# Performance work log

Hardware: AMD Instinct MI355X
Metric: run time of the kernel (lower is better)

The kernel has to match this reference:

```python
import jax, jax.numpy as jnp
import numpy as np

N = 50000      # nodes
E = 400000     # edges (before self-loops)
IN = 256       # in_dim
H = 4          # heads in layer 1
C = 64         # h_dim (per-head channels, layer 1)
OUT = 16       # out_dim (layer 2, 1 head)
NEG_SLOPE = 0.2


def gatv2_layer(x, src, dst, Wl, bl, Wr, br, att, bias, heads, ch, concat, num_nodes):
    # x: [N, F]; src/dst: [E']; Wl/Wr: [F, heads*ch]; att: [heads, ch]
    xl = (x @ Wl + bl).reshape(num_nodes, heads, ch)  # source transform
    xr = (x @ Wr + br).reshape(num_nodes, heads, ch)  # target transform
    m = xl[src] + xr[dst]                              # [E', H, C] gather
    e = jnp.sum(jax.nn.leaky_relu(m, NEG_SLOPE) * att, axis=-1)  # [E', H]
    # segment softmax over incoming edges of each dst node (self-loops ensure non-empty)
    emax = jax.ops.segment_max(e, dst, num_segments=num_nodes)   # [N, H]
    ee = jnp.exp(e - emax[dst])
    denom = jax.ops.segment_sum(ee, dst, num_segments=num_nodes)  # [N, H]
    alpha = ee / (denom[dst] + 1e-16)                              # [E', H]
    out = jax.ops.segment_sum(alpha[..., None] * xl[src], dst, num_segments=num_nodes)  # [N,H,C]
    if concat:
        out = out.reshape(num_nodes, heads * ch)
    else:
        out = out.mean(axis=1)
    return out + bias


def setup_inputs() -> dict:
    key = jax.random.key(0)
    ks = jax.random.split(key, 16)
    s = 0.05
    inp = {
        "x": jax.random.normal(ks[0], (N, IN), jnp.float32),
        "edge_index": jax.random.randint(ks[1], (2, E), 0, N),
        # layer 1 params (in_dim -> heads*h_dim)
        "Wl1": jax.random.normal(ks[2], (IN, H * C), jnp.float32) * s,
        "bl1": jnp.zeros((H * C,), jnp.float32),
        "Wr1": jax.random.normal(ks[3], (IN, H * C), jnp.float32) * s,
        "br1": jnp.zeros((H * C,), jnp.float32),
        "att1": jax.random.normal(ks[4], (H, C), jnp.float32) * s,
        "bias1": jnp.zeros((H * C,), jnp.float32),
        # layer 2 params (heads*h_dim -> out_dim, 1 head)
        "Wl2": jax.random.normal(ks[5], (H * C, OUT), jnp.float32) * s,
        "bl2": jnp.zeros((OUT,), jnp.float32),
        "Wr2": jax.random.normal(ks[6], (H * C, OUT), jnp.float32) * s,
        "br2": jnp.zeros((OUT,), jnp.float32),
        "att2": jax.random.normal(ks[7], (1, OUT), jnp.float32) * s,
        "bias2": jnp.zeros((OUT,), jnp.float32),
    }
    return inp


def reference(x, edge_index, Wl1, bl1, Wr1, br1, att1, bias1, Wl2, bl2, Wr2, br2, att2, bias2):
    # add self loops (PyG GATv2Conv default add_self_loops=True)
    loop = jnp.arange(N, dtype=edge_index.dtype)
    src = jnp.concatenate([edge_index[0], loop])
    dst = jnp.concatenate([edge_index[1], loop])
    h = gatv2_layer(x, src, dst, Wl1, bl1, Wr1, br1, att1, bias1, H, C, True, N)
    h = jnp.tanh(h)
    o = gatv2_layer(h, src, dst, Wl2, bl2, Wr2, br2, att2, bias2, 1, OUT, False, N)
    return o, jax.nn.log_softmax(o, axis=1)
```

## Files before the change

kernel.cpp:

```cpp
#include <hip/hip_runtime.h>

typedef __bf16 bfv8 __attribute__((ext_vector_type(8)));
typedef float f32x4 __attribute__((ext_vector_type(4)));
typedef float f32x2 __attribute__((ext_vector_type(2)));
typedef short shortv8 __attribute__((ext_vector_type(8)));
typedef unsigned short usv8 __attribute__((ext_vector_type(8)));

__device__ __forceinline__ float b2f(unsigned short u) {
  unsigned int v = ((unsigned int)u) << 16;
  float f;
  __builtin_memcpy(&f, &v, 4);
  return f;
}
__device__ __forceinline__ unsigned short f2b(float f) {
  unsigned int u;
  __builtin_memcpy(&u, &f, 4);
  u += 0x7fffu + ((u >> 16) & 1u);
  return (unsigned short)(u >> 16);
}

__device__ __forceinline__ f32x2 bf2x(unsigned int u) {
  f32x2 r;
  r.x = __builtin_bit_cast(float, u << 16);
  r.y = __builtin_bit_cast(float, u & 0xffff0000u);
  return r;
}

template <int CTRL>
__device__ __forceinline__ float dpp_mv(float x) {
  int xi = __builtin_bit_cast(int, x);
  int yi = __builtin_amdgcn_update_dpp(0, xi, CTRL, 0xf, 0xf, true);
  return __builtin_bit_cast(float, yi);
}

__device__ __forceinline__ float tanh_fast(float x) {
  float e2 = __expf(2.f * x);
  float r = __builtin_amdgcn_rcpf(e2 + 1.f);
  float th = fmaf(-2.f, r, 1.f);
  if (!(th == th)) th = 0.f;
  return th;
}

__global__ void probe_kernel(const unsigned short* __restrict__ x, int* __restrict__ flag) {
  int lane = threadIdx.x;
  int cnt = 0;
  for (int i = lane; i < 4096; i += 64) {
    unsigned int e = (x[i] >> 7) & 0xffu;
    if (e >= 0x86u) cnt++;
  }
#pragma unroll
  for (int off = 1; off < 64; off <<= 1) cnt += __shfl_xor(cnt, off, 64);
  if (lane == 0) *flag = (cnt > 100) ? 1 : 0;
}

#define P_TOT 140352
__global__ __launch_bounds__(256) void fused_pre_kernel(
    const void* __restrict__ x, unsigned short* __restrict__ Xc,
    const int* __restrict__ flagp, int NX,
    const int* __restrict__ ei, int E, int Nn, int* __restrict__ cnt,
    const void* p0, const void* p1, const void* p2, const void* p3,
    const void* p4, const void* p5, const void* p6, const void* p7,
    const void* p8, const void* p9, const void* p10, const void* p11,
    unsigned short* __restrict__ Pc, int nb_convx, int nb_count) {
  int b = blockIdx.x;
  int t = threadIdx.x;
  if (b < nb_convx) {
    if (!*flagp) return;
    int i = (b * 256 + t) * 4;
    if (i >= NX) return;
    float4 f = *reinterpret_cast<const float4*>((const float*)x + i);
    ushort4 o;
    o.x = f2b(f.x); o.y = f2b(f.y); o.z = f2b(f.z); o.w = f2b(f.w);
    *reinterpret_cast<ushort4*>(Xc + i) = o;
  } else if (b < nb_convx + nb_count) {
    int i = (b - nb_convx) * 256 + t;
    int total = E + Nn;
    if (i >= total) return;
    int d = (i < E) ? ei[E + i] : (i - E);
    if ((unsigned)d >= (unsigned)Nn) d = 0;
    atomicAdd(&cnt[d], 1);
  } else {
    int i = (b - nb_convx - nb_count) * 256 + t;
    if (i >= P_TOT) return;
    const int offs[13] = {0, 65536, 65792, 131328, 131584, 131840, 132096,
                          136192, 136208, 140304, 140320, 140336, P_TOT};
    const void* ptrs[12] = {p0, p1, p2, p3, p4, p5, p6, p7, p8, p9, p10, p11};
    int flag = *flagp;
    int k = 0;
    while (i >= offs[k + 1]) k++;
    int local = i - offs[k];
    unsigned short v;
    if (flag) v = f2b(((const float*)ptrs[k])[local]);
    else v = ((const unsigned short*)ptrs[k])[local];
    Pc[i] = v;
  }
}

__global__ __launch_bounds__(1024) void fused_mid_kernel(
    const int* __restrict__ cnt, int* __restrict__ row_start, int* __restrict__ blkTot,
    int* __restrict__ cursor, int Nn, int nb_scan,
    const unsigned short* __restrict__ Pc,
    unsigned short* __restrict__ WT1, unsigned short* __restrict__ WT2) {
  int b = blockIdx.x;
  int t = threadIdx.x;
  if (b < nb_scan) {
    __shared__ int buf[1024];
    int i = b * 1024 + t;
    int v = (i < Nn) ? cnt[i] : 0;
    buf[t] = v;
    if (i < Nn) cursor[i] = 0;
    __syncthreads();
    for (int off = 1; off < 1024; off <<= 1) {
      int x = (t >= off) ? buf[t - off] : 0;
      __syncthreads();
      buf[t] += x;
      __syncthreads();
    }
    if (i < Nn) row_start[i] = buf[t] - v;
    if (t == 1023) blkTot[b] = buf[1023];
  } else {
    int idx = (b - nb_scan) * 1024 + t;
    if (idx < 512 * 256) {
      int n = idx >> 8, k = idx & 255;
      WT1[idx] = (n < 256) ? Pc[0 + k * 256 + n]
                           : Pc[65792 + k * 256 + (n - 256)];
    } else {
      int j = idx - 512 * 256;
      if (j < 32 * 256) {
        int n = j >> 8, k = j & 255;
        WT2[j] = (n < 16) ? Pc[132096 + k * 16 + n]
                          : Pc[136208 + k * 16 + (n - 16)];
      }
    }
  }
}

__global__ __launch_bounds__(64) void scan2_kernel(const int* __restrict__ blkTot,
                                                   int* __restrict__ blkOff, int nb,
                                                   int* __restrict__ row_start, int Nn,
                                                   int total) {
  int lane = threadIdx.x;
  int v = (lane < nb) ? blkTot[lane] : 0;
  int s = v;
#pragma unroll
  for (int off = 1; off < 64; off <<= 1) {
    int u = __shfl_up(s, off, 64);
    if (lane >= off) s += u;
  }
  int excl = s - v;
  blkOff[lane] = excl;
  if (lane == 63) blkOff[64] = s;
  int idx = Nn >> 10;
  int bo = (idx >= 64) ? __shfl(s, 63, 64) : __shfl(excl, idx, 64);
  if (lane == 0) row_start[Nn] = total - bo;
}

__global__ __launch_bounds__(256) void fill_kernel(const int* __restrict__ ei, int E, int Nn,
                                                   const int* __restrict__ row_start,
                                                   const int* __restrict__ blkOff,
                                                   int* __restrict__ cursor,
                                                   int* __restrict__ csr_src) {
  int i = blockIdx.x * 256 + threadIdx.x;
  int total = E + Nn;
  if (i >= total) return;
  int s, d;
  if (i < E) { s = ei[i]; d = ei[E + i]; } else { s = i - E; d = i - E; }
  if ((unsigned)d >= (unsigned)Nn) d = 0;
  if ((unsigned)s >= (unsigned)Nn) s = 0;
  int pos = row_start[d] + blkOff[d >> 10] + atomicAdd(&cursor[d], 1);
  if ((unsigned)pos < (unsigned)total) csr_src[pos] = s;
}

__global__ __launch_bounds__(256) void gemm1_kernel(
    const unsigned short* __restrict__ Xc,
    const unsigned short* __restrict__ x_raw,
    const int* __restrict__ flagp,
    const unsigned short* __restrict__ WT,
    const unsigned short* __restrict__ bl, const unsigned short* __restrict__ br,
    unsigned short* __restrict__ C, int M) {
  __shared__ unsigned short smem[16384];
  const unsigned short* X = (*flagp) ? Xc : x_raw;
  const int t = threadIdx.x;
  const int lane = t & 63;
  const int w = t >> 6;
  const int quad = lane >> 4;
  const int l16 = lane & 15;

  const int G = (M + 127) >> 7;
  const int nfull = (G >> 3) << 5;
  int bid = blockIdx.x, grp, n_blk;
  if (bid < nfull) {
    grp = (bid >> 5) * 8 + (bid & 7);
    n_blk = (bid >> 3) & 3;
  } else {
    int r = bid - nfull;
    grp = (G & ~7) + (r >> 2);
    n_blk = r & 3;
  }
  const int m_blk = grp * 128;
  const int m_base = m_blk + (w >> 1) * 64;
  const int n_base = n_blk * 128 + (w & 1) * 64;

  const int st_row = t >> 3;
  const int st_seg = t & 7;

  f32x4 acc[4][4];
#pragma unroll
  for (int i = 0; i < 4; i++)
#pragma unroll
    for (int j = 0; j < 4; j++) acc[i][j] = (f32x4){0.f, 0.f, 0.f, 0.f};

  shortv8 st[4];
#pragma unroll
  for (int i = 0; i < 4; i++) {
    int gr = m_blk + st_row + 32 * i;
    if (gr >= M) gr = M - 1;
    st[i] = *reinterpret_cast<const shortv8*>(X + (size_t)gr * 256 + st_seg * 8);
  }
#pragma unroll
  for (int i = 0; i < 4; i++) {
    int row = st_row + 32 * i;
    *reinterpret_cast<shortv8*>(smem + row * 64 + ((st_seg ^ (row & 7)) * 8)) = st[i];
  }
  __syncthreads();

#pragma unroll
  for (int c = 0; c < 4; c++) {
    if (c < 3) {
#pragma unroll
      for (int i = 0; i < 4; i++) {
        int gr = m_blk + st_row + 32 * i;
        if (gr >= M) gr = M - 1;
        st[i] = *reinterpret_cast<const shortv8*>(X + (size_t)gr * 256 + (c + 1) * 64 +
                                                  st_seg * 8);
      }
    }
    const unsigned short* bb = smem + (c & 1) * 8192;
#pragma unroll
    for (int sub = 0; sub < 2; sub++) {
      bfv8 a[4], b[4];
      int seg_r = sub * 4 + quad;
#pragma unroll
      for (int i = 0; i < 4; i++) {
        int lrow = (w >> 1) * 64 + 16 * i + l16;
        a[i] = *reinterpret_cast<const bfv8*>(bb + lrow * 64 + ((seg_r ^ (lrow & 7)) * 8));
      }
#pragma unroll
      for (int j = 0; j < 4; j++) {
        int col = n_base + 16 * j + l16;
        b[j] = *reinterpret_cast<const bfv8*>(WT + (size_t)col * 256 + c * 64 + sub * 32 +
                                              quad * 8);
      }
#pragma unroll
      for (int i = 0; i < 4; i++)
#pragma unroll
        for (int j = 0; j < 4; j++)
          acc[i][j] = __builtin_amdgcn_mfma_f32_16x16x32_bf16(a[i], b[j], acc[i][j], 0, 0, 0);
    }
    if (c < 3) {
      int buf = (c + 1) & 1;
#pragma unroll
      for (int i = 0; i < 4; i++) {
        int row = st_row + 32 * i;
        *reinterpret_cast<shortv8*>(smem + buf * 8192 + row * 64 +
                                    ((st_seg ^ (row & 7)) * 8)) = st[i];
      }
      __syncthreads();
    }
  }

  __syncthreads();
  unsigned short* lt = smem + w * 2304;
#pragma unroll
  for (int h = 0; h < 2; h++) {
#pragma unroll
    for (int j = 0; j < 4; j++) {
      int col = n_base + 16 * j + l16;
      float bias = (col < 256) ? b2f(bl[col]) : b2f(br[col - 256]);
#pragma unroll
      for (int i2 = 0; i2 < 2; i2++) {
        int i = 2 * h + i2;
#pragma unroll
        for (int r = 0; r < 4; r++)
          lt[(16 * i2 + quad * 4 + r) * 72 + 16 * j + l16] = f2b(acc[i][j][r] + bias);
      }
    }
#pragma unroll
    for (int pass = 0; pass < 4; pass++) {
      int row = pass * 8 + (lane >> 3);
      int colg = (lane & 7) * 8;
      shortv8 v = *reinterpret_cast<const shortv8*>(lt + row * 72 + colg);
      int grow = m_base + 32 * h + row;
      if (grow < M)
        *reinterpret_cast<shortv8*>(C + (size_t)grow * 512 + n_base + colg) = v;
    }
  }
}

__global__ __launch_bounds__(256) void gemm2_kernel(
    const unsigned short* __restrict__ H, const unsigned short* __restrict__ WT,
    const unsigned short* __restrict__ bl, const unsigned short* __restrict__ br,
    float* __restrict__ C, int M) {
  __shared__ unsigned short smem[8192];
  const int t = threadIdx.x;
  const int lane = t & 63;
  const int w = t >> 6;
  const int quad = lane >> 4;
  const int l16 = lane & 15;
  const int m_blk = blockIdx.x * 64;
  const int wrow = w * 16;

  const int st_row = t >> 2;
  const int st_seg = t & 3;

  f32x4 acc[2];
  acc[0] = (f32x4){0.f, 0.f, 0.f, 0.f};
  acc[1] = (f32x4){0.f, 0.f, 0.f, 0.f};

  int gr = m_blk + st_row;
  if (gr >= M) gr = M - 1;
  const unsigned short* hrow = H + (size_t)gr * 256;

  shortv8 st0 = *reinterpret_cast<const shortv8*>(hrow + st_seg * 8);
  shortv8 st1 = *reinterpret_cast<const shortv8*>(hrow + st_seg * 8 + 32);
  *reinterpret_cast<shortv8*>(smem + st_row * 64 + ((st_seg ^ (st_row & 7)) * 8)) = st0;
  *reinterpret_cast<shortv8*>(smem + st_row * 64 + (((st_seg + 4) ^ (st_row & 7)) * 8)) = st1;
  __syncthreads();

#pragma unroll
  for (int c = 0; c < 4; c++) {
    if (c < 3) {
      st0 = *reinterpret_cast<const shortv8*>(hrow + (c + 1) * 64 + st_seg * 8);
      st1 = *reinterpret_cast<const shortv8*>(hrow + (c + 1) * 64 + st_seg * 8 + 32);
    }
    const unsigned short* bb = smem + (c & 1) * 4096;
#pragma unroll
    for (int sub = 0; sub < 2; sub++) {
      int seg_r = sub * 4 + quad;
      int lrow = wrow + l16;
      bfv8 a = *reinterpret_cast<const bfv8*>(bb + lrow * 64 + ((seg_r ^ (lrow & 7)) * 8));
      bfv8 b[2];
#pragma unroll
      for (int j = 0; j < 2; j++) {
        int col = 16 * j + l16;
        b[j] = *reinterpret_cast<const bfv8*>(WT + (size_t)col * 256 + c * 64 + sub * 32 +
                                              quad * 8);
      }
#pragma unroll
      for (int j = 0; j < 2; j++)
        acc[j] = __builtin_amdgcn_mfma_f32_16x16x32_bf16(a, b[j], acc[j], 0, 0, 0);
    }
    if (c < 3) {
      int buf = (c + 1) & 1;
      *reinterpret_cast<shortv8*>(smem + buf * 4096 + st_row * 64 +
                                  ((st_seg ^ (st_row & 7)) * 8)) = st0;
      *reinterpret_cast<shortv8*>(smem + buf * 4096 + st_row * 64 +
                                  (((st_seg + 4) ^ (st_row & 7)) * 8)) = st1;
      __syncthreads();
    }
  }

#pragma unroll
  for (int j = 0; j < 2; j++) {
    int col = 16 * j + l16;
    float bias = (j == 0) ? b2f(bl[l16]) : b2f(br[l16]);
#pragma unroll
    for (int r = 0; r < 4; r++) {
      int row = m_blk + wrow + quad * 4 + r;
      if (row < M) C[(size_t)row * 32 + col] = acc[j][r] + bias;
    }
  }
}

__global__ __launch_bounds__(256) void agg1_kernel(
    const unsigned short* __restrict__ C1,
    const unsigned short* __restrict__ att1,
    const unsigned short* __restrict__ bias1,
    const int* __restrict__ row_start, const int* __restrict__ blkOff,
    const int* __restrict__ csr_src,
    unsigned short* __restrict__ H1,
    int Nn, int Etot) {
  int wid = blockIdx.x * 4 + (threadIdx.x >> 6);
  if (wid >= Nn) return;
  int lane = threadIdx.x & 63;
  int half = lane >> 5;
  int c0 = (lane & 31) * 8;

  f32x2 at2[4], xr2[4];
  {
    uint4 a4 = *reinterpret_cast<const uint4*>(att1 + c0);
    uint4 r4 = *reinterpret_cast<const uint4*>(C1 + (size_t)wid * 512 + 256 + c0);
    at2[0] = bf2x(a4.x); at2[1] = bf2x(a4.y); at2[2] = bf2x(a4.z); at2[3] = bf2x(a4.w);
    xr2[0] = bf2x(r4.x); xr2[1] = bf2x(r4.y); xr2[2] = bf2x(r4.z); xr2[3] = bf2x(r4.w);
  }

  float denom = 0.f;
  f32x2 acc2[4] = {};
  int beg = row_start[wid] + blkOff[wid >> 10];
  int end = row_start[wid + 1] + blkOff[(wid + 1) >> 10];
  if (beg < 0) beg = 0;
  if (end < beg || end - beg > Etot) end = beg;

  for (int base = beg; base < end; base += 64) {
    int cend = min(end, base + 64);
    int pl = base + lane;
    if (pl >= end) pl = end - 1;
    int s_pre = csr_src[pl];
#pragma unroll 4
    for (int i = base; i < cend; i += 2) {
      int p = i + half;
      bool valid = p < cend;
      int s = __shfl(s_pre, p - base, 64);
      if ((unsigned)s >= (unsigned)Nn) s = 0;
      uint4 rw = *reinterpret_cast<const uint4*>(C1 + (size_t)s * 512 + c0);
      f32x2 xl0 = bf2x(rw.x), xl1 = bf2x(rw.y), xl2 = bf2x(rw.z), xl3 = bf2x(rw.w);
      f32x2 m0 = xl0 + xr2[0], m1 = xl1 + xr2[1];
      f32x2 m2 = xl2 + xr2[2], m3 = xl3 + xr2[3];
      f32x2 l0 = __builtin_elementwise_max(m0, m0 * 0.2f);
      f32x2 l1 = __builtin_elementwise_max(m1, m1 * 0.2f);
      f32x2 l2 = __builtin_elementwise_max(m2, m2 * 0.2f);
      f32x2 l3 = __builtin_elementwise_max(m3, m3 * 0.2f);
      f32x2 d2 = l0 * at2[0];
      d2 += l1 * at2[1];
      d2 += l2 * at2[2];
      d2 += l3 * at2[3];
      float dot = d2.x + d2.y;
      dot += dpp_mv<0xB1>(dot);
      dot += dpp_mv<0x4E>(dot);
      dot += dpp_mv<0x141>(dot);
      dot = fminf(fmaxf(dot, -60.f), 60.f);
      float wgt = valid ? __expf(dot) : 0.f;
      denom += wgt;
      acc2[0] += xl0 * wgt;
      acc2[1] += xl1 * wgt;
      acc2[2] += xl2 * wgt;
      acc2[3] += xl3 * wgt;
    }
  }
  denom += __shfl_xor(denom, 32, 64);
#pragma unroll
  for (int k = 0; k < 4; k++) {
    acc2[k].x += __shfl_xor(acc2[k].x, 32, 64);
    acc2[k].y += __shfl_xor(acc2[k].y, 32, 64);
  }

  if (half == 0) {
    float inv = __builtin_amdgcn_rcpf(denom + 1e-16f);
    uint4 b4 = *reinterpret_cast<const uint4*>(bias1 + c0);
    f32x2 bb[4] = {bf2x(b4.x), bf2x(b4.y), bf2x(b4.z), bf2x(b4.w)};
    uint4 o;
    unsigned int od[4];
#pragma unroll
    for (int k = 0; k < 4; k++) {
      f32x2 xv = acc2[k] * inv + bb[k];
      float t0 = tanh_fast(xv.x);
      float t1 = tanh_fast(xv.y);
      od[k] = (unsigned int)f2b(t0) | ((unsigned int)f2b(t1) << 16);
    }
    o.x = od[0]; o.y = od[1]; o.z = od[2]; o.w = od[3];
    *reinterpret_cast<uint4*>(H1 + (size_t)wid * 256 + c0) = o;
  }
}

__global__ __launch_bounds__(256) void agg2_kernel(
    const float* __restrict__ C2,
    const unsigned short* __restrict__ att2,
    const unsigned short* __restrict__ bias2,
    const int* __restrict__ row_start, const int* __restrict__ blkOff,
    const int* __restrict__ csr_src,
    float* __restrict__ out,
    int Nn, int Etot) {
  int wid = blockIdx.x * 4 + (threadIdx.x >> 6);
  if (wid >= Nn) return;
  int lane = threadIdx.x & 63;
  int eslot = lane >> 2;
  int cg = (lane & 3) * 4;

  float at[4], xr[4];
  {
    ushort4 a4 = *reinterpret_cast<const ushort4*>(att2 + cg);
    at[0] = b2f(a4.x); at[1] = b2f(a4.y); at[2] = b2f(a4.z); at[3] = b2f(a4.w);
    float4 r4 = *reinterpret_cast<const float4*>(C2 + (size_t)wid * 32 + 16 + cg);
    xr[0] = r4.x; xr[1] = r4.y; xr[2] = r4.z; xr[3] = r4.w;
  }

  float denom = 0.f;
  float acc[4] = {0.f, 0.f, 0.f, 0.f};
  int beg = row_start[wid] + blkOff[wid >> 10];
  int end = row_start[wid + 1] + blkOff[(wid + 1) >> 10];
  if (beg < 0) beg = 0;
  if (end < beg || end - beg > Etot) end = beg;

  for (int base = beg; base < end; base += 64) {
    int cend = min(end, base + 64);
    int pl = base + lane;
    if (pl >= end) pl = end - 1;
    int s_pre = csr_src[pl];
    for (int i = base; i < cend; i += 16) {
      int p = i + eslot;
      bool valid = p < cend;
      int s = __shfl(s_pre, p - base, 64);
      if ((unsigned)s >= (unsigned)Nn) s = 0;
      float4 x4 = *reinterpret_cast<const float4*>(C2 + (size_t)s * 32 + cg);
      float xl[4] = {x4.x, x4.y, x4.z, x4.w};
      float dot = 0.f;
#pragma unroll
      for (int k = 0; k < 4; k++) {
        float m = xl[k] + xr[k];
        float l = fmaxf(m, 0.2f * m);
        dot = fmaf(l, at[k], dot);
      }
      dot += dpp_mv<0xB1>(dot);
      dot += dpp_mv<0x4E>(dot);
      dot = fminf(fmaxf(dot, -60.f), 60.f);
      float wgt = valid ? __expf(dot) : 0.f;
      denom += wgt;
#pragma unroll
      for (int k = 0; k < 4; k++) acc[k] = fmaf(wgt, xl[k], acc[k]);
    }
  }
  denom += dpp_mv<0x124>(denom);
  denom += dpp_mv<0x128>(denom);
#pragma unroll
  for (int k = 0; k < 4; k++) {
    acc[k] += dpp_mv<0x124>(acc[k]);
    acc[k] += dpp_mv<0x128>(acc[k]);
  }
#pragma unroll
  for (int off = 16; off <= 32; off <<= 1) {
    denom += __shfl_xor(denom, off, 64);
#pragma unroll
    for (int k = 0; k < 4; k++) acc[k] += __shfl_xor(acc[k], off, 64);
  }

  float inv = __builtin_amdgcn_rcpf(denom + 1e-16f);
  ushort4 b4 = *reinterpret_cast<const ushort4*>(bias2 + cg);
  float bb[4] = {b2f(b4.x), b2f(b4.y), b2f(b4.z), b2f(b4.w)};
  float o[4];
#pragma unroll
  for (int k = 0; k < 4; k++) {
    o[k] = acc[k] * inv + bb[k];
    if (!(o[k] == o[k])) o[k] = 0.f;
  }
  float mx = fmaxf(fmaxf(o[0], o[1]), fmaxf(o[2], o[3]));
  mx = fmaxf(mx, dpp_mv<0xB1>(mx));
  mx = fmaxf(mx, dpp_mv<0x4E>(mx));
  float se = 0.f;
#pragma unroll
  for (int k = 0; k < 4; k++) se += __expf(o[k] - mx);
  se += dpp_mv<0xB1>(se);
  se += dpp_mv<0x4E>(se);
  float ls = logf(se);
  if (lane < 4) {
    float4 vo = {o[0], o[1], o[2], o[3]};
    float4 vl = {o[0] - mx - ls, o[1] - mx - ls, o[2] - mx - ls, o[3] - mx - ls};
    *reinterpret_cast<float4*>(out + (size_t)wid * 16 + cg) = vo;
    *reinterpret_cast<float4*>(out + (size_t)Nn * 16 + (size_t)wid * 16 + cg) = vl;
  }
}

extern "C" void kernel_launch(void* const* d_in, const int* in_sizes, int n_in,
                              void* d_out, int out_size, void* d_ws, size_t ws_size,
                              hipStream_t stream) {
  const void* x_raw = d_in[0];
  const int* ei     = (const int*)d_in[1];

  const int M = in_sizes[0] / 256;
  const int E = in_sizes[1] / 2;
  const int TOT = E + M;
  const int NX = M * 256;

  char* ws = (char*)d_ws;
  size_t off = 0;
  auto alloc = [&](size_t bytes) -> void* {
    void* p = ws + off;
    off = (off + bytes + 255) & ~(size_t)255;
    return p;
  };
  int*            flag   = (int*)alloc(4);
  unsigned short* Pc     = (unsigned short*)alloc((size_t)P_TOT * 2);
  unsigned short* Xc     = (unsigned short*)alloc((size_t)NX * 2);
  unsigned short* WT1    = (unsigned short*)alloc((size_t)512 * 256 * 2);
  unsigned short* WT2    = (unsigned short*)alloc((size_t)32 * 256 * 2);
  int*            cnt    = (int*)alloc((size_t)M * 4);
  int*            cursor = (int*)alloc((size_t)M * 4);
  int*            row_start = (int*)alloc((size_t)(M + 1) * 4);
  int*            csr_src   = (int*)alloc((size_t)TOT * 4);
  int*            blkTot = (int*)alloc(64 * 4);
  int*            blkOff = (int*)alloc(65 * 4);
  float*          C2     = (float*)alloc((size_t)M * 32 * 4);
  unsigned short* C1     = (unsigned short*)alloc((size_t)M * 512 * 2);
  const size_t need = off;
  (void)n_in;
  unsigned short* H1 = Xc;

  if (ws_size < need) {
    hipMemsetAsync(d_out, 0, (size_t)out_size * 4, stream);
    return;
  }

  unsigned short* bl1c   = Pc + 65536;
  unsigned short* br1c   = Pc + 131328;
  unsigned short* att1c  = Pc + 131584;
  unsigned short* bias1c = Pc + 131840;
  unsigned short* bl2c   = Pc + 136192;
  unsigned short* br2c   = Pc + 140304;
  unsigned short* att2c  = Pc + 140320;
  unsigned short* bias2c = Pc + 140336;

  hipMemsetAsync(cnt, 0, (size_t)M * 4, stream);

  probe_kernel<<<1, 64, 0, stream>>>((const unsigned short*)x_raw, flag);

  const int nb_convx = (NX / 4 + 255) / 256;
  const int nb_count = (TOT + 255) / 256;
  const int nb_convp = (P_TOT + 255) / 256;
  fused_pre_kernel<<<nb_convx + nb_count + nb_convp, 256, 0, stream>>>(
      x_raw, Xc, flag, NX, ei, E, M, cnt,
      d_in[2], d_in[3], d_in[4], d_in[5], d_in[6], d_in[7], d_in[8], d_in[9],
      d_in[10], d_in[11], d_in[12], d_in[13], Pc, nb_convx, nb_count);

  const int nb_scan = (M + 1023) / 1024;
  const int nb_tr = (512 * 256 + 32 * 256 + 1023) / 1024;
  fused_mid_kernel<<<nb_scan + nb_tr, 1024, 0, stream>>>(cnt, row_start, blkTot,
                                                         cursor, M, nb_scan, Pc, WT1, WT2);

  scan2_kernel<<<1, 64, 0, stream>>>(blkTot, blkOff, nb_scan, row_start, M, TOT);

  fill_kernel<<<(TOT + 255) / 256, 256, 0, stream>>>(ei, E, M, row_start, blkOff,
                                                     cursor, csr_src);

  const int nb_gemm = 4 * ((M + 127) / 128);
  gemm1_kernel<<<nb_gemm, 256, 0, stream>>>(Xc, (const unsigned short*)x_raw, flag,
                                            WT1, bl1c, br1c, C1, M);

  agg1_kernel<<<(M + 3) / 4, 256, 0, stream>>>(C1, att1c, bias1c, row_start, blkOff,
                                               csr_src, H1, M, TOT);

  gemm2_kernel<<<(M + 63) / 64, 256, 0, stream>>>(H1, WT2, bl2c, br2c, C2, M);

  agg2_kernel<<<(M + 3) / 4, 256, 0, stream>>>(C2, att2c, bias2c, row_start, blkOff,
                                               csr_src, (float*)d_out, M, TOT);
}
```

Before: 284.4 us.

## Retile layer-1 GEMM to 64-row full-width blocks and widen agg1 lanes

The layer-1 GEMM now uses 64-row blocks in which each wave computes 64x128 of the full 512-wide output. This drops the grouped swizzled 128x128 tiling, so each X row is loaded once per block instead of four times across N-blocks, at the cost of more accumulator registers (128 floats per lane). The agg1 kernel now processes 4 edges per iteration with 16 lanes per edge, each lane covering 16 channels, so the per-edge dot reduction takes one fewer DPP step and more gathers are in flight. This raises register pressure and may reduce occupancy in both kernels.

```diff
diff --git a/kernel.cpp b/kernel.cpp
--- a/kernel.cpp
+++ b/kernel.cpp
@@ -178,75 +178,53 @@
     const unsigned short* __restrict__ WT,
     const unsigned short* __restrict__ bl, const unsigned short* __restrict__ br,
     unsigned short* __restrict__ C, int M) {
-  __shared__ unsigned short smem[16384];
+  __shared__ unsigned short smem[8704];
   const unsigned short* X = (*flagp) ? Xc : x_raw;
   const int t = threadIdx.x;
   const int lane = t & 63;
   const int w = t >> 6;
   const int quad = lane >> 4;
   const int l16 = lane & 15;
-
-  const int G = (M + 127) >> 7;
-  const int nfull = (G >> 3) << 5;
-  int bid = blockIdx.x, grp, n_blk;
-  if (bid < nfull) {
-    grp = (bid >> 5) * 8 + (bid & 7);
-    n_blk = (bid >> 3) & 3;
-  } else {
-    int r = bid - nfull;
-    grp = (G & ~7) + (r >> 2);
-    n_blk = r & 3;
-  }
-  const int m_blk = grp * 128;
-  const int m_base = m_blk + (w >> 1) * 64;
-  const int n_base = n_blk * 128 + (w & 1) * 64;
-
-  const int st_row = t >> 3;
-  const int st_seg = t & 7;
-
-  f32x4 acc[4][4];
+  const int m_blk = blockIdx.x * 64;
+  const int n_base = w * 128;
+
+  const int st_row = t >> 2;
+  const int st_seg = t & 3;
+
+  f32x4 acc[4][8];
 #pragma unroll
   for (int i = 0; i < 4; i++)
 #pragma unroll
-    for (int j = 0; j < 4; j++) acc[i][j] = (f32x4){0.f, 0.f, 0.f, 0.f};
-
-  shortv8 st[4];
-#pragma unroll
-  for (int i = 0; i < 4; i++) {
-    int gr = m_blk + st_row + 32 * i;
-    if (gr >= M) gr = M - 1;
-    st[i] = *reinterpret_cast<const shortv8*>(X + (size_t)gr * 256 + st_seg * 8);
-  }
-#pragma unroll
-  for (int i = 0; i < 4; i++) {
-    int row = st_row + 32 * i;
-    *reinterpret_cast<shortv8*>(smem + row * 64 + ((st_seg ^ (row & 7)) * 8)) = st[i];
-  }
+    for (int j = 0; j < 8; j++) acc[i][j] = (f32x4){0.f, 0.f, 0.f, 0.f};
+
+  int gr = m_blk + st_row;
+  if (gr >= M) gr = M - 1;
+  const unsigned short* xrow = X + (size_t)gr * 256;
+
+  shortv8 st0 = *reinterpret_cast<const shortv8*>(xrow + st_seg * 8);
+  shortv8 st1 = *reinterpret_cast<const shortv8*>(xrow + st_seg * 8 + 32);
+  *reinterpret_cast<shortv8*>(smem + st_row * 64 + ((st_seg ^ (st_row & 7)) * 8)) = st0;
+  *reinterpret_cast<shortv8*>(smem + st_row * 64 + (((st_seg + 4) ^ (st_row & 7)) * 8)) = st1;
   __syncthreads();
 
 #pragma unroll
   for (int c = 0; c < 4; c++) {
     if (c < 3) {
+      st0 = *reinterpret_cast<const shortv8*>(xrow + (c + 1) * 64 + st_seg * 8);
+      st1 = *reinterpret_cast<const shortv8*>(xrow + (c + 1) * 64 + st_seg * 8 + 32);
+    }
+    const unsigned short* bb = smem + (c & 1) * 4096;
+#pragma unroll
+    for (int sub = 0; sub < 2; sub++) {
+      int seg_r = sub * 4 + quad;
+      bfv8 a[4], b[8];
 #pragma unroll
       for (int i = 0; i < 4; i++) {
-        int gr = m_blk + st_row + 32 * i;
-        if (gr >= M) gr = M - 1;
-        st[i] = *reinterpret_cast<const shortv8*>(X + (size_t)gr * 256 + (c + 1) * 64 +
-                                                  st_seg * 8);
-      }
-    }
-    const unsigned short* bb = smem + (c & 1) * 8192;
-#pragma unroll
-    for (int sub = 0; sub < 2; sub++) {
-      bfv8 a[4], b[4];
-      int seg_r = sub * 4 + quad;
-#pragma unroll
-      for (int i = 0; i < 4; i++) {
-        int lrow = (w >> 1) * 64 + 16 * i + l16;
+        int lrow = 16 * i + l16;
         a[i] = *reinterpret_cast<const bfv8*>(bb + lrow * 64 + ((seg_r ^ (lrow & 7)) * 8));
       }
 #pragma unroll
-      for (int j = 0; j < 4; j++) {
+      for (int j = 0; j < 8; j++) {
         int col = n_base + 16 * j + l16;
         b[j] = *reinterpret_cast<const bfv8*>(WT + (size_t)col * 256 + c * 64 + sub * 32 +
                                               quad * 8);
@@ -254,43 +232,37 @@
 #pragma unroll
       for (int i = 0; i < 4; i++)
 #pragma unroll
-        for (int j = 0; j < 4; j++)
+        for (int j = 0; j < 8; j++)
           acc[i][j] = __builtin_amdgcn_mfma_f32_16x16x32_bf16(a[i], b[j], acc[i][j], 0, 0, 0);
     }
     if (c < 3) {
       int buf = (c + 1) & 1;
-#pragma unroll
-      for (int i = 0; i < 4; i++) {
-        int row = st_row + 32 * i;
-        *reinterpret_cast<shortv8*>(smem + buf * 8192 + row * 64 +
-                                    ((st_seg ^ (row & 7)) * 8)) = st[i];
-      }
+      *reinterpret_cast<shortv8*>(smem + buf * 4096 + st_row * 64 +
+                                  ((st_seg ^ (st_row & 7)) * 8)) = st0;
+      *reinterpret_cast<shortv8*>(smem + buf * 4096 + st_row * 64 +
+                                  (((st_seg + 4) ^ (st_row & 7)) * 8)) = st1;
       __syncthreads();
     }
   }
 
   __syncthreads();
-  unsigned short* lt = smem + w * 2304;
-#pragma unroll
-  for (int h = 0; h < 2; h++) {
-#pragma unroll
-    for (int j = 0; j < 4; j++) {
+  unsigned short* lt = smem + w * 2176;
+#pragma unroll
+  for (int i = 0; i < 4; i++) {
+#pragma unroll
+    for (int j = 0; j < 8; j++) {
       int col = n_base + 16 * j + l16;
       float bias = (col < 256) ? b2f(bl[col]) : b2f(br[col - 256]);
 #pragma unroll
-      for (int i2 = 0; i2 < 2; i2++) {
-        int i = 2 * h + i2;
-#pragma unroll
-        for (int r = 0; r < 4; r++)
-          lt[(16 * i2 + quad * 4 + r) * 72 + 16 * j + l16] = f2b(acc[i][j][r] + bias);
-      }
+      for (int r = 0; r < 4; r++)
+        lt[(quad * 4 + r) * 136 + 16 * j + l16] = f2b(acc[i][j][r] + bias);
     }
 #pragma unroll
     for (int pass = 0; pass < 4; pass++) {
-      int row = pass * 8 + (lane >> 3);
-      int colg = (lane & 7) * 8;
-      shortv8 v = *reinterpret_cast<const shortv8*>(lt + row * 72 + colg);
-      int grow = m_base + 32 * h + row;
+      int row = pass * 4 + (lane >> 4);
+      int colg = (lane & 15) * 8;
+      shortv8 v = *reinterpret_cast<const shortv8*>(lt + row * 136 + colg);
+      int grow = m_blk + 16 * i + row;
       if (grow < M)
         *reinterpret_cast<shortv8*>(C + (size_t)grow * 512 + n_base + colg) = v;
     }
@@ -383,19 +355,23 @@
   int wid = blockIdx.x * 4 + (threadIdx.x >> 6);
   if (wid >= Nn) return;
   int lane = threadIdx.x & 63;
-  int half = lane >> 5;
-  int c0 = (lane & 31) * 8;
-
-  f32x2 at2[4], xr2[4];
+  int g = lane >> 4;
+  int c0 = (lane & 15) * 16;
+
+  f32x2 at2[8], xr2[8];
   {
     uint4 a4 = *reinterpret_cast<const uint4*>(att1 + c0);
+    uint4 a5 = *reinterpret_cast<const uint4*>(att1 + c0 + 8);
     uint4 r4 = *reinterpret_cast<const uint4*>(C1 + (size_t)wid * 512 + 256 + c0);
+    uint4 r5 = *reinterpret_cast<const uint4*>(C1 + (size_t)wid * 512 + 256 + c0 + 8);
     at2[0] = bf2x(a4.x); at2[1] = bf2x(a4.y); at2[2] = bf2x(a4.z); at2[3] = bf2x(a4.w);
+    at2[4] = bf2x(a5.x); at2[5] = bf2x(a5.y); at2[6] = bf2x(a5.z); at2[7] = bf2x(a5.w);
     xr2[0] = bf2x(r4.x); xr2[1] = bf2x(r4.y); xr2[2] = bf2x(r4.z); xr2[3] = bf2x(r4.w);
+    xr2[4] = bf2x(r5.x); xr2[5] = bf2x(r5.y); xr2[6] = bf2x(r5.z); xr2[7] = bf2x(r5.w);
   }
 
   float denom = 0.f;
-  f32x2 acc2[4] = {};
+  f32x2 acc2[8] = {};
   int beg = row_start[wid] + blkOff[wid >> 10];
   int end = row_start[wid + 1] + blkOff[(wid + 1) >> 10];
   if (beg < 0) beg = 0;
@@ -406,59 +382,63 @@
     int pl = base + lane;
     if (pl >= end) pl = end - 1;
     int s_pre = csr_src[pl];
-#pragma unroll 4
-    for (int i = base; i < cend; i += 2) {
-      int p = i + half;
+#pragma unroll 2
+    for (int i = base; i < cend; i += 4) {
+      int p = i + g;
       bool valid = p < cend;
       int s = __shfl(s_pre, p - base, 64);
       if ((unsigned)s >= (unsigned)Nn) s = 0;
-      uint4 rw = *reinterpret_cast<const uint4*>(C1 + (size_t)s * 512 + c0);
-      f32x2 xl0 = bf2x(rw.x), xl1 = bf2x(rw.y), xl2 = bf2x(rw.z), xl3 = bf2x(rw.w);
-      f32x2 m0 = xl0 + xr2[0], m1 = xl1 + xr2[1];
-      f32x2 m2 = xl2 + xr2[2], m3 = xl3 + xr2[3];
-      f32x2 l0 = __builtin_elementwise_max(m0, m0 * 0.2f);
-      f32x2 l1 = __builtin_elementwise_max(m1, m1 * 0.2f);
-      f32x2 l2 = __builtin_elementwise_max(m2, m2 * 0.2f);
-      f32x2 l3 = __builtin_elementwise_max(m3, m3 * 0.2f);
-      f32x2 d2 = l0 * at2[0];
-      d2 += l1 * at2[1];
-      d2 += l2 * at2[2];
-      d2 += l3 * at2[3];
+      const unsigned short* row = C1 + (size_t)s * 512 + c0;
+      uint4 ra = *reinterpret_cast<const uint4*>(row);
+      uint4 rb = *reinterpret_cast<const uint4*>(row + 8);
+      f32x2 xl[8];
+      xl[0] = bf2x(ra.x); xl[1] = bf2x(ra.y); xl[2] = bf2x(ra.z); xl[3] = bf2x(ra.w);
+      xl[4] = bf2x(rb.x); xl[5] = bf2x(rb.y); xl[6] = bf2x(rb.z); xl[7] = bf2x(rb.w);
+      f32x2 d2 = {0.f, 0.f};
+#pragma unroll
+      for (int k = 0; k < 8; k++) {
+        f32x2 m = xl[k] + xr2[k];
+        f32x2 l = __builtin_elementwise_max(m, m * 0.2f);
+        d2 += l * at2[k];
+      }
       float dot = d2.x + d2.y;
       dot += dpp_mv<0xB1>(dot);
       dot += dpp_mv<0x4E>(dot);
-      dot += dpp_mv<0x141>(dot);
       dot = fminf(fmaxf(dot, -60.f), 60.f);
       float wgt = valid ? __expf(dot) : 0.f;
       denom += wgt;
-      acc2[0] += xl0 * wgt;
-      acc2[1] += xl1 * wgt;
-      acc2[2] += xl2 * wgt;
-      acc2[3] += xl3 * wgt;
-    }
-  }
-  denom += __shfl_xor(denom, 32, 64);
-#pragma unroll
-  for (int k = 0; k < 4; k++) {
-    acc2[k].x += __shfl_xor(acc2[k].x, 32, 64);
-    acc2[k].y += __shfl_xor(acc2[k].y, 32, 64);
-  }
-
-  if (half == 0) {
+#pragma unroll
+      for (int k = 0; k < 8; k++) acc2[k] += xl[k] * wgt;
+    }
+  }
+#pragma unroll
+  for (int off = 16; off <= 32; off <<= 1) {
+    denom += __shfl_xor(denom, off, 64);
+#pragma unroll
+    for (int k = 0; k < 8; k++) {
+      acc2[k].x += __shfl_xor(acc2[k].x, off, 64);
+      acc2[k].y += __shfl_xor(acc2[k].y, off, 64);
+    }
+  }
+
+  if (g == 0) {
     float inv = __builtin_amdgcn_rcpf(denom + 1e-16f);
     uint4 b4 = *reinterpret_cast<const uint4*>(bias1 + c0);
-    f32x2 bb[4] = {bf2x(b4.x), bf2x(b4.y), bf2x(b4.z), bf2x(b4.w)};
-    uint4 o;
-    unsigned int od[4];
-#pragma unroll
-    for (int k = 0; k < 4; k++) {
+    uint4 b5 = *reinterpret_cast<const uint4*>(bias1 + c0 + 8);
+    f32x2 bb[8] = {bf2x(b4.x), bf2x(b4.y), bf2x(b4.z), bf2x(b4.w),
+                   bf2x(b5.x), bf2x(b5.y), bf2x(b5.z), bf2x(b5.w)};
+    unsigned int od[8];
+#pragma unroll
+    for (int k = 0; k < 8; k++) {
       f32x2 xv = acc2[k] * inv + bb[k];
       float t0 = tanh_fast(xv.x);
       float t1 = tanh_fast(xv.y);
       od[k] = (unsigned int)f2b(t0) | ((unsigned int)f2b(t1) << 16);
     }
-    o.x = od[0]; o.y = od[1]; o.z = od[2]; o.w = od[3];
-    *reinterpret_cast<uint4*>(H1 + (size_t)wid * 256 + c0) = o;
+    uint4 o0 = {od[0], od[1], od[2], od[3]};
+    uint4 o1 = {od[4], od[5], od[6], od[7]};
+    *reinterpret_cast<uint4*>(H1 + (size_t)wid * 256 + c0) = o0;
+    *reinterpret_cast<uint4*>(H1 + (size_t)wid * 256 + c0 + 8) = o1;
   }
 }
 
@@ -630,9 +610,8 @@
   fill_kernel<<<(TOT + 255) / 256, 256, 0, stream>>>(ei, E, M, row_start, blkOff,
                                                      cursor, csr_src);
 
-  const int nb_gemm = 4 * ((M + 127) / 128);
-  gemm1_kernel<<<nb_gemm, 256, 0, stream>>>(Xc, (const unsigned short*)x_raw, flag,
-                                            WT1, bl1c, br1c, C1, M);
+  gemm1_kernel<<<(M + 63) / 64, 256, 0, stream>>>(Xc, (const unsigned short*)x_raw, flag,
+                                                  WT1, bl1c, br1c, C1, M);
 
   agg1_kernel<<<(M + 3) / 4, 256, 0, stream>>>(C1, att1c, bias1c, row_start, blkOff,
                                                csr_src, H1, M, TOT);
```

Result: slower. 316.4 us (+11.2%).

## Fold dtype probe into pre kernel and block-offset scan into fill kernel

Applied to the files above, without the earlier changes.

Removes the standalone probe kernel: each conversion and parameter block now recomputes the dtype-detection probe itself, and block 0 writes the flag for later kernels. The tiny scan2 kernel is merged into fill_kernel, where every wavefront redoes the 64-entry block-offset scan and fetches the offset with a shuffle instead of a global load. This cuts two launches and their serialization gaps at the cost of redundant per-block reads and reductions. It also lowers the unroll factor of the layer-1 aggregation edge loop.

```diff
diff --git a/kernel.cpp b/kernel.cpp
--- a/kernel.cpp
+++ b/kernel.cpp
@@ -41,31 +41,41 @@
   return th;
 }
 
-__global__ void probe_kernel(const unsigned short* __restrict__ x, int* __restrict__ flag) {
-  int lane = threadIdx.x;
+__device__ __forceinline__ int block_probe(const unsigned short* __restrict__ xs,
+                                           int* __restrict__ red) {
+  int t = threadIdx.x;
+  const uint4* p = reinterpret_cast<const uint4*>(xs) + t * 2;
+  uint4 a = p[0], b = p[1];
+  unsigned int w[8] = {a.x, a.y, a.z, a.w, b.x, b.y, b.z, b.w};
   int cnt = 0;
-  for (int i = lane; i < 4096; i += 64) {
-    unsigned int e = (x[i] >> 7) & 0xffu;
-    if (e >= 0x86u) cnt++;
+#pragma unroll
+  for (int k = 0; k < 8; k++) {
+    if ((((w[k] & 0xffffu) >> 7) & 0xffu) >= 0x86u) cnt++;
+    if (((w[k] >> 23) & 0xffu) >= 0x86u) cnt++;
   }
 #pragma unroll
   for (int off = 1; off < 64; off <<= 1) cnt += __shfl_xor(cnt, off, 64);
-  if (lane == 0) *flag = (cnt > 100) ? 1 : 0;
+  if ((t & 63) == 0) red[t >> 6] = cnt;
+  __syncthreads();
+  return (red[0] + red[1] + red[2] + red[3]) > 100 ? 1 : 0;
 }
 
 #define P_TOT 140352
 __global__ __launch_bounds__(256) void fused_pre_kernel(
     const void* __restrict__ x, unsigned short* __restrict__ Xc,
-    const int* __restrict__ flagp, int NX,
+    int* __restrict__ flagw, int NX,
     const int* __restrict__ ei, int E, int Nn, int* __restrict__ cnt,
     const void* p0, const void* p1, const void* p2, const void* p3,
     const void* p4, const void* p5, const void* p6, const void* p7,
     const void* p8, const void* p9, const void* p10, const void* p11,
     unsigned short* __restrict__ Pc, int nb_convx, int nb_count) {
+  __shared__ int red[4];
   int b = blockIdx.x;
   int t = threadIdx.x;
   if (b < nb_convx) {
-    if (!*flagp) return;
+    int flag = block_probe((const unsigned short*)x, red);
+    if (b == 0 && t == 0) *flagw = flag;
+    if (!flag) return;
     int i = (b * 256 + t) * 4;
     if (i >= NX) return;
     float4 f = *reinterpret_cast<const float4*>((const float*)x + i);
@@ -80,12 +90,12 @@
     if ((unsigned)d >= (unsigned)Nn) d = 0;
     atomicAdd(&cnt[d], 1);
   } else {
+    int flag = block_probe((const unsigned short*)x, red);
     int i = (b - nb_convx - nb_count) * 256 + t;
     if (i >= P_TOT) return;
     const int offs[13] = {0, 65536, 65792, 131328, 131584, 131840, 132096,
                           136192, 136208, 140304, 140320, 140336, P_TOT};
     const void* ptrs[12] = {p0, p1, p2, p3, p4, p5, p6, p7, p8, p9, p10, p11};
-    int flag = *flagp;
     int k = 0;
     while (i >= offs[k + 1]) k++;
     int local = i - offs[k];
@@ -135,12 +145,15 @@
   }
 }
 
-__global__ __launch_bounds__(64) void scan2_kernel(const int* __restrict__ blkTot,
-                                                   int* __restrict__ blkOff, int nb,
-                                                   int* __restrict__ row_start, int Nn,
-                                                   int total) {
-  int lane = threadIdx.x;
-  int v = (lane < nb) ? blkTot[lane] : 0;
+__global__ __launch_bounds__(256) void fill_kernel(const int* __restrict__ ei, int E, int Nn,
+                                                   int* __restrict__ row_start,
+                                                   const int* __restrict__ blkTot, int nbscan,
+                                                   int* __restrict__ cursor,
+                                                   int* __restrict__ csr_src,
+                                                   int* __restrict__ blkOff) {
+  int lane = threadIdx.x & 63;
+  int total = E + Nn;
+  int v = (lane < nbscan) ? blkTot[lane] : 0;
   int s = v;
 #pragma unroll
   for (int off = 1; off < 64; off <<= 1) {
@@ -148,27 +161,28 @@
     if (lane >= off) s += u;
   }
   int excl = s - v;
-  blkOff[lane] = excl;
-  if (lane == 63) blkOff[64] = s;
-  int idx = Nn >> 10;
-  int bo = (idx >= 64) ? __shfl(s, 63, 64) : __shfl(excl, idx, 64);
-  if (lane == 0) row_start[Nn] = total - bo;
-}
-
-__global__ __launch_bounds__(256) void fill_kernel(const int* __restrict__ ei, int E, int Nn,
-                                                   const int* __restrict__ row_start,
-                                                   const int* __restrict__ blkOff,
-                                                   int* __restrict__ cursor,
-                                                   int* __restrict__ csr_src) {
+
+  if (blockIdx.x == 0 && threadIdx.x < 64) {
+    blkOff[lane] = excl;
+    if (lane == 63) blkOff[64] = s;
+    int idx = Nn >> 10;
+    int bo = (idx >= 64) ? __shfl(s, 63, 64) : __shfl(excl, idx, 64);
+    if (lane == 0) row_start[Nn] = total - bo;
+  }
+
   int i = blockIdx.x * 256 + threadIdx.x;
-  int total = E + Nn;
-  if (i >= total) return;
-  int s, d;
-  if (i < E) { s = ei[i]; d = ei[E + i]; } else { s = i - E; d = i - E; }
-  if ((unsigned)d >= (unsigned)Nn) d = 0;
-  if ((unsigned)s >= (unsigned)Nn) s = 0;
-  int pos = row_start[d] + blkOff[d >> 10] + atomicAdd(&cursor[d], 1);
-  if ((unsigned)pos < (unsigned)total) csr_src[pos] = s;
+  bool act = i < total;
+  int sv = 0, d = 0;
+  if (act) {
+    if (i < E) { sv = ei[i]; d = ei[E + i]; } else { sv = i - E; d = i - E; }
+    if ((unsigned)d >= (unsigned)Nn) d = 0;
+    if ((unsigned)sv >= (unsigned)Nn) sv = 0;
+  }
+  int bo_d = __shfl(excl, d >> 10, 64);
+  if (act) {
+    int pos = row_start[d] + bo_d + atomicAdd(&cursor[d], 1);
+    if ((unsigned)pos < (unsigned)total) csr_src[pos] = sv;
+  }
 }
 
 __global__ __launch_bounds__(256) void gemm1_kernel(
@@ -406,7 +420,7 @@
     int pl = base + lane;
     if (pl >= end) pl = end - 1;
     int s_pre = csr_src[pl];
-#pragma unroll 4
+#pragma unroll 2
     for (int i = base; i < cend; i += 2) {
       int p = i + half;
       bool valid = p < cend;
@@ -610,8 +624,6 @@
 
   hipMemsetAsync(cnt, 0, (size_t)M * 4, stream);
 
-  probe_kernel<<<1, 64, 0, stream>>>((const unsigned short*)x_raw, flag);
-
   const int nb_convx = (NX / 4 + 255) / 256;
   const int nb_count = (TOT + 255) / 256;
   const int nb_convp = (P_TOT + 255) / 256;
@@ -625,10 +637,8 @@
   fused_mid_kernel<<<nb_scan + nb_tr, 1024, 0, stream>>>(cnt, row_start, blkTot,
                                                          cursor, M, nb_scan, Pc, WT1, WT2);
 
-  scan2_kernel<<<1, 64, 0, stream>>>(blkTot, blkOff, nb_scan, row_start, M, TOT);
-
-  fill_kernel<<<(TOT + 255) / 256, 256, 0, stream>>>(ei, E, M, row_start, blkOff,
-                                                     cursor, csr_src);
+  fill_kernel<<<(TOT + 255) / 256, 256, 0, stream>>>(ei, E, M, row_start, blkTot,
+                                                     nb_scan, cursor, csr_src, blkOff);
 
   const int nb_gemm = 4 * ((M + 127) / 128);
   gemm1_kernel<<<nb_gemm, 256, 0, stream>>>(Xc, (const unsigned short*)x_raw, flag,
```

Measured after the change: 275.3 us (median of 2 runs). -3.2%, faster.
